# Optimization experiments

Measured on AMD Instinct MI355X. Metric: run time of the kernel, lower is better.

Reference implementation:

```python
import jax, jax.numpy as jnp
import numpy as np

PAD = 50
CLUSTERING_WEIGHT = 1.0
SAMPLE_NUMBER = 8192
EPS = 1e-6


def setup_inputs() -> dict:
    key = jax.random.key(0)
    k1, k2 = jax.random.split(key)
    n, c, h, w = 2, 19, 512, 512
    output = jax.random.uniform(k1, (n, c, h, w), dtype=jnp.float32)
    hw_cropped = (h - 2 * PAD) * (w - 2 * PAD)  # 412*412 = 169744
    sample = jax.random.randint(k2, (SAMPLE_NUMBER,), 0, hw_cropped, dtype=jnp.int64)
    return {"output": output, "sample": sample}


def reference(output, sample):
    n, c, h, w = output.shape
    # crop pad border
    out = output[:, :, PAD:h - PAD, PAD:w - PAD]  # [n, c, h', w']
    prob = out.reshape(n, c, -1)[:, :, sample]     # [n, c, S]
    prob_t = jnp.swapaxes(prob, 1, 2)              # [n, S, c]
    # sampled similarity: [n, S, S] (memory-heavy intermediate)
    sim = jnp.einsum('nsc,ntc->nst', prob_t, prob_t)
    ind = jnp.argmax(sim, axis=2)                  # [n, S]
    # nearest[b, i, k] = prob_t[b, ind[b, i], k]
    nearest = jnp.take_along_axis(prob_t, ind[:, :, None], axis=1)  # [n, S, c]
    # robust_crossentropy(pred=prob_t, tgt=nearest)
    loss = -(nearest * jnp.log(prob_t + EPS))
    loss = loss.mean() * CLUSTERING_WEIGHT
    return loss[None]  # shape [1]
```

## Files before the change

### kernel.cpp

```cpp
#include <hip/hip_runtime.h>
#include <math.h>

#define N 2
#define C 19
#define H 512
#define W 512
#define PADC 50
#define WC 412
#define S 8192
#define CP 20
#define XP 64
#define NCHUNK 16
#define CHUNKT (S / NCHUNK)
#define TTS 128
#define NSTG (CHUNKT / TTS)
#define TPS (TTS / 32)
#define LPITCH 72
#define NBLK ((N * S) / 8)
#define EPSF 1e-6f

typedef __attribute__((ext_vector_type(8))) short short8;
typedef __attribute__((ext_vector_type(16))) float f32x16;

__device__ __forceinline__ unsigned short f2bf_rne(float x) {
    unsigned u = __float_as_uint(x);
    unsigned r = (u + 0x7FFFu + ((u >> 16) & 1u)) >> 16;
    return (unsigned short)r;
}
__device__ __forceinline__ float bf2f(unsigned short h) {
    return __uint_as_float(((unsigned)h) << 16);
}
__device__ __forceinline__ float max3f(float a, float b, float c) {
    float d;
    asm("v_max3_f32 %0, %1, %2, %3" : "=v"(d) : "v"(a), "v"(b), "v"(c));
    return d;
}
__device__ __forceinline__ float max3f_c0(float a, float b) {
    float d;
    asm("v_max3_f32 %0, %1, %2, 0" : "=v"(d) : "v"(a), "v"(b));
    return d;
}
__device__ __forceinline__ float max16c(const f32x16 a) {
    float m0 = max3f(a[0],  a[1],  a[2]);
    float m1 = max3f(a[3],  a[4],  a[5]);
    float m2 = max3f(a[6],  a[7],  a[8]);
    float m3 = max3f(a[9],  a[10], a[11]);
    float m4 = max3f(a[12], a[13], a[14]);
    float n0 = max3f(m0, m1, m2);
    float n1 = max3f(m3, m4, a[15]);
    return max3f_c0(n0, n1);
}

__global__ void gather_k(const float* __restrict__ out4d,
                         const int* __restrict__ sample,
                         float* __restrict__ P32,
                         unsigned short* __restrict__ XA,
                         unsigned short* __restrict__ XB) {
    int idx = blockIdx.x * blockDim.x + threadIdx.x;
    int lane = idx & 63;
    int hi   = lane >> 5;
    int l    = lane & 31;
    int ns = idx >> 5;
    int nn = ns >> 13;
    int s  = ns & (S - 1);
    int smp = sample[s];
    int row = smp / WC;
    int col = smp - row * WC;
    const float* base = out4d + ((size_t)nn * C) * H * W
                      + (size_t)(PADC + row) * W + (PADC + col);
    float v = 0.f;
    if (l < C) v = base[(size_t)l * (H * W)];
    unsigned hb = f2bf_rne(v);
    unsigned lb = f2bf_rne(v - bf2f((unsigned short)hb));

    if (l < CP) P32[(size_t)ns * CP + l] = v;

    int base32 = hi << 5;
    int srcA = base32 + (l < C ? l : l - C);
    int srcB = base32 + (l < C ? l : l - 6);
    unsigned lbA = (unsigned)__shfl((int)lb, srcA, 64);
    unsigned hbA = (unsigned)__shfl((int)hb, srcA, 64);
    unsigned lbB = (unsigned)__shfl((int)lb, srcB, 64);
    unsigned hbB = (unsigned)__shfl((int)hb, srcB, 64);

    unsigned short a0 = (unsigned short)(l < C ? hb : lbA);
    unsigned short a1 = (unsigned short)(l < C ? hb : (l < 25 ? lbB : 0u));
    unsigned short b0 = (unsigned short)hbA;
    unsigned short b1 = (unsigned short)(l < C ? lb : (l < 25 ? hbB : 0u));

    unsigned short* xa = XA + (size_t)ns * XP;
    unsigned short* xb = XB + (size_t)ns * XP;
    xa[l]      = a0;
    xa[32 + l] = a1;
    xb[l]      = b0;
    xb[32 + l] = b1;
}

__global__ __launch_bounds__(256, 4) void argmax_k(const unsigned short* __restrict__ XA,
                                                   const unsigned short* __restrict__ XB,
                                                   unsigned* __restrict__ keys) {
    __shared__ unsigned short lds[2][TTS * LPITCH];
    int b = blockIdx.x;
    int chunk  = b & (NCHUNK - 1);
    int sgroup = (b >> 4) & 31;
    int nn     = b >> 9;
    int tid  = threadIdx.x;
    int w    = tid >> 6;
    int lane = tid & 63;
    int col  = lane & 31;
    int hi   = lane >> 5;
    int s0   = sgroup * 256 + w * 32;
    int s1   = s0 + 128;
    int t0   = chunk * CHUNKT;
    const unsigned short* XAn = XA + (size_t)nn * S * XP;
    const unsigned short* XBn = XB + (size_t)nn * S * XP;

    short8 bfA[4], bfB[4];
    {
        const unsigned short* ba = XBn + (size_t)(s0 + col) * XP + hi * 8;
        bfA[0] = *(const short8*)(ba);      bfA[1] = *(const short8*)(ba + 16);
        bfA[2] = *(const short8*)(ba + 32); bfA[3] = *(const short8*)(ba + 48);
        const unsigned short* bb = XBn + (size_t)(s1 + col) * XP + hi * 8;
        bfB[0] = *(const short8*)(bb);      bfB[1] = *(const short8*)(bb + 16);
        bfB[2] = *(const short8*)(bb + 32); bfB[3] = *(const short8*)(bb + 48);
    }

    f32x16 zacc = {};
    unsigned kA = 0u, kB = 0u;

    {
        const float4* src = (const float4*)(XAn + (size_t)t0 * XP);
        #pragma unroll
        for (int k = 0; k < 4; ++k) {
            int f = k * 256 + tid;
            *(float4*)(&lds[0][(f >> 3) * LPITCH + (f & 7) * 8]) = src[f];
        }
    }
    __syncthreads();

    int cur = 0;
    for (int st = 0; st < NSTG; ++st) {
        float4 nx[4];
        if (st + 1 < NSTG) {
            const float4* srcn = (const float4*)(XAn + (size_t)(t0 + (st + 1) * TTS) * XP);
            #pragma unroll
            for (int k = 0; k < 4; ++k) nx[k] = srcn[k * 256 + tid];
        }
        const unsigned short* bs = &lds[cur][0];
        #pragma unroll
        for (int ts = 0; ts < TPS; ++ts) {
            const unsigned short* arow = bs + (ts * 32 + col) * LPITCH + hi * 8;
            short8 a0 = *(const short8*)(arow);
            short8 a1 = *(const short8*)(arow + 16);
            short8 a2 = *(const short8*)(arow + 32);
            short8 a3 = *(const short8*)(arow + 48);
            f32x16 accA = __builtin_amdgcn_mfma_f32_32x32x16_bf16(a0, bfA[0], zacc, 0, 0, 0);
            accA = __builtin_amdgcn_mfma_f32_32x32x16_bf16(a1, bfA[1], accA, 0, 0, 0);
            accA = __builtin_amdgcn_mfma_f32_32x32x16_bf16(a2, bfA[2], accA, 0, 0, 0);
            accA = __builtin_amdgcn_mfma_f32_32x32x16_bf16(a3, bfA[3], accA, 0, 0, 0);
            f32x16 accB = __builtin_amdgcn_mfma_f32_32x32x16_bf16(a0, bfB[0], zacc, 0, 0, 0);
            accB = __builtin_amdgcn_mfma_f32_32x32x16_bf16(a1, bfB[1], accB, 0, 0, 0);
            accB = __builtin_amdgcn_mfma_f32_32x32x16_bf16(a2, bfB[2], accB, 0, 0, 0);
            accB = __builtin_amdgcn_mfma_f32_32x32x16_bf16(a3, bfB[3], accB, 0, 0, 0);
            int tile = st * TPS + ts;
            unsigned tb = (unsigned)(63 - tile);
            unsigned vA = (__float_as_uint(max16c(accA)) & ~63u) | tb;
            unsigned vB = (__float_as_uint(max16c(accB)) & ~63u) | tb;
            kA = kA > vA ? kA : vA;
            kB = kB > vB ? kB : vB;
        }
        if (st + 1 < NSTG) {
            #pragma unroll
            for (int k = 0; k < 4; ++k) {
                int f = k * 256 + tid;
                *(float4*)(&lds[cur ^ 1][(f >> 3) * LPITCH + (f & 7) * 8]) = nx[k];
            }
        }
        __syncthreads();
        cur ^= 1;
    }

    unsigned oA = __shfl(kA, lane ^ 32, 64);
    unsigned oB = __shfl(kB, lane ^ 32, 64);
    kA = kA > oA ? kA : oA;
    kB = kB > oB ? kB : oB;
    if (lane < 32) {
        size_t basek = ((size_t)nn * NCHUNK + chunk) * S;
        keys[basek + s0 + col] = kA;
        keys[basek + s1 + col] = kB;
    }
}

__global__ __launch_bounds__(256) void refine_loss_k(const float* __restrict__ P32,
                                                     const unsigned* __restrict__ keys,
                                                     float* __restrict__ bsum) {
    __shared__ float red[8];
    int tid = threadIdx.x;
    int lane = tid & 63;
    int hi = lane >> 5;
    int l  = lane & 31;
    int ns = blockIdx.x * 8 + (tid >> 6) * 2 + hi;
    int nn = ns >> 13;
    int s  = ns & (S - 1);

    int cl = l & (NCHUNK - 1);
    unsigned k = keys[((size_t)nn * NCHUNK + cl) * S + s];
    unsigned long long key64 = ((unsigned long long)(k >> 6) << 32)
                             | (unsigned)((((NCHUNK - 1) - cl) << 6) | (k & 63u));
    #pragma unroll
    for (int off = 16; off > 0; off >>= 1) {
        unsigned long long o = __shfl_xor(key64, off, 32);
        key64 = o > key64 ? o : key64;
    }
    int bc    = (NCHUNK - 1) - (int)((key64 >> 6) & (NCHUNK - 1));
    int tile  = 63 - (int)(key64 & 63);
    int tbase = bc * CHUNKT + tile * 32;

    const float* Pn = P32 + (size_t)nn * S * CP;
    const float* sr = Pn + (size_t)s * CP;
    const float* tr = Pn + (size_t)(tbase + l) * CP;
    float v = 0.f;
    #pragma unroll
    for (int c = 0; c < C; ++c) v = fmaf(sr[c], tr[c], v);
    int t = tbase + l;
    #pragma unroll
    for (int off = 16; off > 0; off >>= 1) {
        float ov = __shfl_xor(v, off, 32);
        int   ot = __shfl_xor(t, off, 32);
        if (ov > v || (ov == v && ot < t)) { v = ov; t = ot; }
    }
    const float* nrow = Pn + (size_t)t * CP;
    float term = 0.f;
    if (l < C) term = -nrow[l] * logf(sr[l] + EPSF);
    #pragma unroll
    for (int off = 16; off > 0; off >>= 1)
        term += __shfl_xor(term, off, 32);
    if (l == 0) red[tid >> 5] = term;
    __syncthreads();
    if (tid == 0) {
        float a = 0.f;
        #pragma unroll
        for (int i = 0; i < 8; ++i) a += red[i];
        bsum[blockIdx.x] = a;
    }
}

__global__ __launch_bounds__(256) void final_k(const float* __restrict__ bsum,
                                               float* __restrict__ out) {
    __shared__ float red[256];
    int tid = threadIdx.x;
    float a = 0.f;
    #pragma unroll
    for (int i = 0; i < NBLK / 256; ++i) a += bsum[i * 256 + tid];
    red[tid] = a;
    __syncthreads();
    for (int off = 128; off > 0; off >>= 1) {
        if (tid < off) red[tid] += red[tid + off];
        __syncthreads();
    }
    if (tid == 0) out[0] = red[0] / (float)(N * S * C);
}

extern "C" void kernel_launch(void* const* d_in, const int* in_sizes, int n_in,
                              void* d_out, int out_size, void* d_ws, size_t ws_size,
                              hipStream_t stream) {
    const float* out4d  = (const float*)d_in[0];
    const int*   sample = (const int*)d_in[1];

    float*          P32  = (float*)d_ws;
    unsigned short* XA   = (unsigned short*)(P32 + (size_t)N * S * CP);
    unsigned short* XB   = XA + (size_t)N * S * XP;
    unsigned*       keys = (unsigned*)(XB + (size_t)N * S * XP);
    float*          bsum = (float*)(keys + (size_t)N * NCHUNK * S);
    float*          outp = (float*)d_out;

    gather_k<<<(N * S * 32) / 256, 256, 0, stream>>>(out4d, sample, P32, XA, XB);
    argmax_k<<<N * 32 * NCHUNK, 256, 0, stream>>>(XA, XB, keys);
    refine_loss_k<<<NBLK, 256, 0, stream>>>(P32, keys, bsum);
    final_k<<<1, 256, 0, stream>>>(bsum, outp);
}
```

Baseline: 35.61 us.

## Widen argmax tile to four query column blocks per wave, use 32 chunks

Each wave now holds B fragments for four 32-row query blocks instead of two, so every A tile loaded from LDS feeds twice as many MFMAs. To keep the block count the same, the target dimension is split into 32 chunks instead of 16, and refine_loss_k now reduces one key per lane across all 32 chunks. The larger register footprint lowers the launch bound to 3 blocks per CU, and the keys buffer doubles in size.

```diff
diff --git a/kernel.cpp b/kernel.cpp
--- a/kernel.cpp
+++ b/kernel.cpp
@@ -10,7 +10,7 @@
 #define S 8192
 #define CP 20
 #define XP 64
-#define NCHUNK 16
+#define NCHUNK 32
 #define CHUNKT (S / NCHUNK)
 #define TTS 128
 #define NSTG (CHUNKT / TTS)
@@ -96,37 +96,39 @@
     xb[32 + l] = b1;
 }
 
-__global__ __launch_bounds__(256, 4) void argmax_k(const unsigned short* __restrict__ XA,
+__global__ __launch_bounds__(256, 3) void argmax_k(const unsigned short* __restrict__ XA,
                                                    const unsigned short* __restrict__ XB,
                                                    unsigned* __restrict__ keys) {
     __shared__ unsigned short lds[2][TTS * LPITCH];
     int b = blockIdx.x;
     int chunk  = b & (NCHUNK - 1);
-    int sgroup = (b >> 4) & 31;
+    int sgroup = (b >> 5) & 15;
     int nn     = b >> 9;
     int tid  = threadIdx.x;
     int w    = tid >> 6;
     int lane = tid & 63;
     int col  = lane & 31;
     int hi   = lane >> 5;
-    int s0   = sgroup * 256 + w * 32;
-    int s1   = s0 + 128;
     int t0   = chunk * CHUNKT;
     const unsigned short* XAn = XA + (size_t)nn * S * XP;
     const unsigned short* XBn = XB + (size_t)nn * S * XP;
 
-    short8 bfA[4], bfB[4];
-    {
-        const unsigned short* ba = XBn + (size_t)(s0 + col) * XP + hi * 8;
-        bfA[0] = *(const short8*)(ba);      bfA[1] = *(const short8*)(ba + 16);
-        bfA[2] = *(const short8*)(ba + 32); bfA[3] = *(const short8*)(ba + 48);
-        const unsigned short* bb = XBn + (size_t)(s1 + col) * XP + hi * 8;
-        bfB[0] = *(const short8*)(bb);      bfB[1] = *(const short8*)(bb + 16);
-        bfB[2] = *(const short8*)(bb + 32); bfB[3] = *(const short8*)(bb + 48);
+    int sb[4];
+    short8 bf[4][4];
+    #pragma unroll
+    for (int j = 0; j < 4; ++j) {
+        sb[j] = sgroup * 512 + (w * 4 + j) * 32;
+        const unsigned short* bp = XBn + (size_t)(sb[j] + col) * XP + hi * 8;
+        bf[j][0] = *(const short8*)(bp);
+        bf[j][1] = *(const short8*)(bp + 16);
+        bf[j][2] = *(const short8*)(bp + 32);
+        bf[j][3] = *(const short8*)(bp + 48);
+        asm volatile("" : "+v"(bf[j][0]), "+v"(bf[j][1]),
+                          "+v"(bf[j][2]), "+v"(bf[j][3]));
     }
 
     f32x16 zacc = {};
-    unsigned kA = 0u, kB = 0u;
+    unsigned key[4] = {0u, 0u, 0u, 0u};
 
     {
         const float4* src = (const float4*)(XAn + (size_t)t0 * XP);
@@ -154,20 +156,17 @@
             short8 a1 = *(const short8*)(arow + 16);
             short8 a2 = *(const short8*)(arow + 32);
             short8 a3 = *(const short8*)(arow + 48);
-            f32x16 accA = __builtin_amdgcn_mfma_f32_32x32x16_bf16(a0, bfA[0], zacc, 0, 0, 0);
-            accA = __builtin_amdgcn_mfma_f32_32x32x16_bf16(a1, bfA[1], accA, 0, 0, 0);
-            accA = __builtin_amdgcn_mfma_f32_32x32x16_bf16(a2, bfA[2], accA, 0, 0, 0);
-            accA = __builtin_amdgcn_mfma_f32_32x32x16_bf16(a3, bfA[3], accA, 0, 0, 0);
-            f32x16 accB = __builtin_amdgcn_mfma_f32_32x32x16_bf16(a0, bfB[0], zacc, 0, 0, 0);
-            accB = __builtin_amdgcn_mfma_f32_32x32x16_bf16(a1, bfB[1], accB, 0, 0, 0);
-            accB = __builtin_amdgcn_mfma_f32_32x32x16_bf16(a2, bfB[2], accB, 0, 0, 0);
-            accB = __builtin_amdgcn_mfma_f32_32x32x16_bf16(a3, bfB[3], accB, 0, 0, 0);
             int tile = st * TPS + ts;
             unsigned tb = (unsigned)(63 - tile);
-            unsigned vA = (__float_as_uint(max16c(accA)) & ~63u) | tb;
-            unsigned vB = (__float_as_uint(max16c(accB)) & ~63u) | tb;
-            kA = kA > vA ? kA : vA;
-            kB = kB > vB ? kB : vB;
+            #pragma unroll
+            for (int j = 0; j < 4; ++j) {
+                f32x16 acc = __builtin_amdgcn_mfma_f32_32x32x16_bf16(a0, bf[j][0], zacc, 0, 0, 0);
+                acc = __builtin_amdgcn_mfma_f32_32x32x16_bf16(a1, bf[j][1], acc, 0, 0, 0);
+                acc = __builtin_amdgcn_mfma_f32_32x32x16_bf16(a2, bf[j][2], acc, 0, 0, 0);
+                acc = __builtin_amdgcn_mfma_f32_32x32x16_bf16(a3, bf[j][3], acc, 0, 0, 0);
+                unsigned v = (__float_as_uint(max16c(acc)) & ~63u) | tb;
+                key[j] = key[j] > v ? key[j] : v;
+            }
         }
         if (st + 1 < NSTG) {
             #pragma unroll
@@ -180,14 +179,12 @@
         cur ^= 1;
     }
 
-    unsigned oA = __shfl(kA, lane ^ 32, 64);
-    unsigned oB = __shfl(kB, lane ^ 32, 64);
-    kA = kA > oA ? kA : oA;
-    kB = kB > oB ? kB : oB;
-    if (lane < 32) {
-        size_t basek = ((size_t)nn * NCHUNK + chunk) * S;
-        keys[basek + s0 + col] = kA;
-        keys[basek + s1 + col] = kB;
+    size_t basek = ((size_t)nn * NCHUNK + chunk) * S;
+    #pragma unroll
+    for (int j = 0; j < 4; ++j) {
+        unsigned o = __shfl(key[j], lane ^ 32, 64);
+        unsigned k = key[j] > o ? key[j] : o;
+        if (lane < 32) keys[basek + sb[j] + col] = k;
     }
 }
 
@@ -203,16 +200,15 @@
     int nn = ns >> 13;
     int s  = ns & (S - 1);
 
-    int cl = l & (NCHUNK - 1);
-    unsigned k = keys[((size_t)nn * NCHUNK + cl) * S + s];
+    unsigned k = keys[((size_t)nn * NCHUNK + l) * S + s];
     unsigned long long key64 = ((unsigned long long)(k >> 6) << 32)
-                             | (unsigned)((((NCHUNK - 1) - cl) << 6) | (k & 63u));
+                             | (unsigned)(((31 - l) << 6) | (k & 63u));
     #pragma unroll
     for (int off = 16; off > 0; off >>= 1) {
         unsigned long long o = __shfl_xor(key64, off, 32);
         key64 = o > key64 ? o : key64;
     }
-    int bc    = (NCHUNK - 1) - (int)((key64 >> 6) & (NCHUNK - 1));
+    int bc    = 31 - (int)((key64 >> 6) & 31);
     int tile  = 63 - (int)(key64 & 63);
     int tbase = bc * CHUNKT + tile * 32;
 
@@ -275,7 +271,7 @@
     float*          outp = (float*)d_out;
 
     gather_k<<<(N * S * 32) / 256, 256, 0, stream>>>(out4d, sample, P32, XA, XB);
-    argmax_k<<<N * 32 * NCHUNK, 256, 0, stream>>>(XA, XB, keys);
+    argmax_k<<<N * 16 * NCHUNK, 256, 0, stream>>>(XA, XB, keys);
     refine_loss_k<<<NBLK, 256, 0, stream>>>(P32, keys, bsum);
     final_k<<<1, 256, 0, stream>>>(bsum, outp);
 }
```

New measurement: 40.39 us. +13.4%, slower.
